# Performance work log

Hardware: AMD Instinct MI355X
Metric: run time of the kernel (lower is better)

Reference implementation:

```python
import jax, jax.numpy as jnp
import numpy as np

TOTAL_WORDS = 10000
EMBED = 100
SEQ = 80
UNITS = 512
BATCH = 2048


def setup_inputs() -> dict:
    key = jax.random.key(0)
    ks = jax.random.split(key, 12)
    s = lambda k, shape, fan: jax.random.normal(k, shape, jnp.float32) * (1.0 / np.sqrt(fan))
    return {
        "tokens": jax.random.randint(ks[0], (BATCH, SEQ), 0, TOTAL_WORDS),
        "emb": jax.random.normal(ks[1], (TOTAL_WORDS, EMBED), jnp.float32) * 0.05,
        "Wx0": s(ks[2], (EMBED, UNITS), EMBED), "Wh0": s(ks[3], (UNITS, UNITS), UNITS), "b0": jnp.zeros((UNITS,), jnp.float32),
        "Wx1": s(ks[4], (UNITS, UNITS), UNITS), "Wh1": s(ks[5], (UNITS, UNITS), UNITS), "b1": jnp.zeros((UNITS,), jnp.float32),
        "Wx2": s(ks[6], (UNITS, UNITS), UNITS), "Wh2": s(ks[7], (UNITS, UNITS), UNITS), "b2": jnp.zeros((UNITS,), jnp.float32),
        "Wout": s(ks[8], (UNITS, 1), UNITS), "bout": jnp.zeros((1,), jnp.float32),
    }


def reference(tokens, emb, Wx0, Wh0, b0, Wx1, Wh1, b1, Wx2, Wh2, b2, Wout, bout):
    # embedding lookup: [B, S, E]
    x = emb[tokens]
    xs = jnp.swapaxes(x, 0, 1)  # [S, B, E] for scan over time
    B = tokens.shape[0]
    h0 = jnp.zeros((B, UNITS), jnp.float32)
    init = (h0, h0, h0)

    def step(carry, word):
        s0, s1, s2 = carry
        o0 = jnp.tanh(word @ Wx0 + s0 @ Wh0 + b0)
        o1 = jnp.tanh(o0 @ Wx1 + s1 @ Wh1 + b1)
        o2 = jnp.tanh(o1 @ Wx2 + s2 @ Wh2 + b2)
        return (o0, o1, o2), None

    (s0, s1, s2), _ = jax.lax.scan(step, init, xs)
    logits = s2 @ Wout + bout  # [B, 1]
    return jax.nn.sigmoid(logits)
```

## Files before the change

kernel.cpp:

```cpp
#include <hip/hip_runtime.h>

#define TW    10000
#define EMBD  100
#define SEQ   80
#define U     512
#define BATCH 2048
#define RPB   16
#define NBLK  (BATCH / RPB)
#define NTHR  1024

typedef short short8 __attribute__((ext_vector_type(8)));
typedef float f32x4 __attribute__((ext_vector_type(4)));

static __device__ __forceinline__ unsigned short f2bf(float f){
  unsigned int u = __float_as_uint(f);
  u += 0x7fffu + ((u >> 16) & 1u);
  return (unsigned short)(u >> 16);
}
static __device__ __forceinline__ float bf2f(unsigned short h){
  return __uint_as_float(((unsigned int)h) << 16);
}
static __device__ __forceinline__ float fast_tanh(float x){
  float e = __expf(2.0f * x);
  return 1.0f - 2.0f / (e + 1.0f);
}

__global__ void proj_kernel(const float* __restrict__ emb, const float* __restrict__ Wx0,
                            const float* __restrict__ b0, float* __restrict__ proj){
  __shared__ float es[16][EMBD];
  const int w0 = blockIdx.x * 16;
  for (int i = threadIdx.x; i < 16 * EMBD; i += 256)
    es[i / EMBD][i % EMBD] = emb[(size_t)w0 * EMBD + i];
  __syncthreads();
  const int n = threadIdx.x;
  float accA[16], accB[16];
#pragma unroll
  for (int wi = 0; wi < 16; ++wi){ accA[wi] = 0.0f; accB[wi] = 0.0f; }
  for (int e = 0; e < EMBD; ++e){
    const float wv0 = Wx0[(size_t)e * U + n];
    const float wv1 = Wx0[(size_t)e * U + n + 256];
#pragma unroll
    for (int wi = 0; wi < 16; ++wi){
      accA[wi] += es[wi][e] * wv0;
      accB[wi] += es[wi][e] * wv1;
    }
  }
  const float bb0 = b0[n], bb1 = b0[n + 256];
  for (int wi = 0; wi < 16; ++wi){
    proj[(size_t)(w0 + wi) * U + n]       = accA[wi] + bb0;
    proj[(size_t)(w0 + wi) * U + n + 256] = accB[wi] + bb1;
  }
}

__global__ void pack_frag(const float* __restrict__ src, unsigned short* __restrict__ dst,
                          int K, int kOff, int NCH){
  const int idx = blockIdx.x * 256 + threadIdx.x;
  if (idx >= K * 512) return;
  const int k = idx / 512, n = idx % 512;
  const int wid = n >> 5, t = (n >> 4) & 1, c = n & 15;
  const int kk = k + kOff;
  const int ch = kk >> 5, khi = (kk >> 3) & 3, j = kk & 7;
  const size_t di = (size_t)wid * NCH * 1024 + (size_t)ch * 1024
                  + (size_t)t * 512 + (size_t)(khi * 16 + c) * 8 + j;
  dst[di] = f2bf(src[(size_t)k * 512 + n]);
}

template<int NCH>
static __device__ __forceinline__ void run_segment(
    const unsigned short* __restrict__ Wp,
    unsigned lofs,
    const unsigned short* __restrict__ stA0, const unsigned short* __restrict__ stA1,
    int aBase, int aSwz, f32x4* acc)
{
#pragma unroll 8
  for (int ch = 0; ch < NCH; ++ch){
    const unsigned short* sA = (NCH == 16 || ch < 16) ? stA0 : stA1;
    short8 a  = *reinterpret_cast<const short8*>(&sA[(aBase + (ch & 15) * 32) ^ aSwz]);
    short8 b0 = *reinterpret_cast<const short8*>(Wp + (unsigned)(ch * 1024) + lofs);
    short8 b1 = *reinterpret_cast<const short8*>(Wp + (unsigned)(ch * 1024 + 512) + lofs);
    acc[0] = __builtin_amdgcn_mfma_f32_16x16x32_bf16(a, b0, acc[0], 0, 0, 0);
    acc[1] = __builtin_amdgcn_mfma_f32_16x16x32_bf16(a, b1, acc[1], 0, 0, 0);
  }
}

__global__ __launch_bounds__(NTHR, 4)
void rnn_persist(const int* __restrict__ tokens,
                 const float* __restrict__ proj,
                 const unsigned short* __restrict__ P0,
                 const unsigned short* __restrict__ P1,
                 const unsigned short* __restrict__ P2,
                 const float* __restrict__ b1,
                 const float* __restrict__ b2,
                 const float* __restrict__ Wout,
                 const float* __restrict__ bout,
                 float* __restrict__ out)
{
  __shared__ unsigned short st0[RPB * U];
  __shared__ unsigned short st1[RPB * U];
  __shared__ unsigned short st2[RPB * U];

  const int tid = threadIdx.x;
  for (int i = tid; i < RPB * U; i += NTHR){ st0[i] = 0; st1[i] = 0; st2[i] = 0; }
  __syncthreads();

  const int lane = tid & 63;
  const int wid  = tid >> 6;
  const int l15  = lane & 15;
  const int khi  = lane >> 4;
  const int n0   = wid * 32;
  const int rowbase = blockIdx.x * RPB;

  const int aBase = l15 * U + khi * 8;
  const int aSwz  = (l15 & 7) << 3;

  const unsigned short* w0p = P0 + (size_t)wid * 16 * 1024;
  const unsigned short* w1p = P1 + (size_t)wid * 32 * 1024;
  const unsigned short* w2p = P2 + (size_t)wid * 32 * 1024;
  const unsigned lofs = (unsigned)lane * 8;

  const int col0 = n0 + l15;
  const int col1 = n0 + 16 + l15;
  const float b1v0 = b1[col0], b1v1 = b1[col1];
  const float b2v0 = b2[col0], b2v1 = b2[col1];

  f32x4 acc[2];

  for (int t = 0; t < SEQ; ++t){
    acc[0] = 0.0f; acc[1] = 0.0f;
    run_segment<16>(w0p, lofs, st0, st0, aBase, aSwz, acc);
    __syncthreads();
    {
      const int rr0 = khi * 4;
#pragma unroll
      for (int j = 0; j < 4; ++j){
        const int rr = rr0 + j;
        const int tk = tokens[(size_t)(rowbase + rr) * SEQ + t];
        const float z0 = acc[0][j] + proj[(size_t)tk * U + col0];
        const float z1 = acc[1][j] + proj[(size_t)tk * U + col1];
        st0[(rr * U + col0) ^ ((rr & 7) << 3)] = f2bf(fast_tanh(z0));
        st0[(rr * U + col1) ^ ((rr & 7) << 3)] = f2bf(fast_tanh(z1));
      }
    }
    __syncthreads();

    acc[0] = 0.0f; acc[1] = 0.0f;
    run_segment<32>(w1p, lofs, st0, st1, aBase, aSwz, acc);
    __syncthreads();
    {
      const int rr0 = khi * 4;
#pragma unroll
      for (int j = 0; j < 4; ++j){
        const int rr = rr0 + j;
        st1[(rr * U + col0) ^ ((rr & 7) << 3)] = f2bf(fast_tanh(acc[0][j] + b1v0));
        st1[(rr * U + col1) ^ ((rr & 7) << 3)] = f2bf(fast_tanh(acc[1][j] + b1v1));
      }
    }
    __syncthreads();

    acc[0] = 0.0f; acc[1] = 0.0f;
    run_segment<32>(w2p, lofs, st1, st2, aBase, aSwz, acc);
    __syncthreads();
    {
      const int rr0 = khi * 4;
#pragma unroll
      for (int j = 0; j < 4; ++j){
        const int rr = rr0 + j;
        st2[(rr * U + col0) ^ ((rr & 7) << 3)] = f2bf(fast_tanh(acc[0][j] + b2v0));
        st2[(rr * U + col1) ^ ((rr & 7) << 3)] = f2bf(fast_tanh(acc[1][j] + b2v1));
      }
    }
    __syncthreads();
  }

  if (wid < RPB){
    const int r = wid;
    float v = 0.0f;
#pragma unroll
    for (int jj = 0; jj < 8; ++jj){
      const int n = lane + jj * 64;
      v += bf2f(st2[(r * U + n) ^ ((r & 7) << 3)]) * Wout[n];
    }
#pragma unroll
    for (int off = 32; off > 0; off >>= 1)
      v += __shfl_down(v, off, 64);
    if (lane == 0)
      out[rowbase + r] = 1.0f / (1.0f + __expf(-(v + bout[0])));
  }
}

extern "C" void kernel_launch(void* const* d_in, const int* in_sizes, int n_in,
                              void* d_out, int out_size, void* d_ws, size_t ws_size,
                              hipStream_t stream){
  (void)in_sizes; (void)n_in; (void)out_size; (void)ws_size;
  const int*   tokens = (const int*)  d_in[0];
  const float* emb  = (const float*)d_in[1];
  const float* Wx0  = (const float*)d_in[2];
  const float* Wh0  = (const float*)d_in[3];
  const float* b0   = (const float*)d_in[4];
  const float* Wx1  = (const float*)d_in[5];
  const float* Wh1  = (const float*)d_in[6];
  const float* b1   = (const float*)d_in[7];
  const float* Wx2  = (const float*)d_in[8];
  const float* Wh2  = (const float*)d_in[9];
  const float* b2   = (const float*)d_in[10];
  const float* Wout = (const float*)d_in[11];
  const float* bout = (const float*)d_in[12];

  char* ws = (char*)d_ws;
  float* proj = (float*)ws;
  unsigned short* P0 = (unsigned short*)(ws + (size_t)TW * U * 4);
  unsigned short* P1 = P0 + (size_t)16 * 16 * 1024;
  unsigned short* P2 = P1 + (size_t)16 * 32 * 1024;

  proj_kernel<<<TW / 16, 256, 0, stream>>>(emb, Wx0, b0, proj);
  const int pblk = (U * U + 255) / 256;
  pack_frag<<<pblk, 256, 0, stream>>>(Wh0, P0, U, 0, 16);
  pack_frag<<<pblk, 256, 0, stream>>>(Wx1, P1, U, 0, 32);
  pack_frag<<<pblk, 256, 0, stream>>>(Wh1, P1, U, U, 32);
  pack_frag<<<pblk, 256, 0, stream>>>(Wx2, P2, U, 0, 32);
  pack_frag<<<pblk, 256, 0, stream>>>(Wh2, P2, U, U, 32);

  rnn_persist<<<NBLK, NTHR, 0, stream>>>(tokens, proj, P0, P1, P2,
                                         b1, b2, Wout, bout, (float*)d_out);
}
```

Measured before the change: 1.796 ms.

## Double-buffer recurrent state in LDS to cut barriers per timestep

Each layer's hidden state gets ping-pong LDS buffers (read the previous step's buffer, write the other), moved to dynamic shared memory. This drops the per-timestep barriers from six to two, since writes no longer race with reads of the same buffer. Token and embedding-projection gathers are issued before the layer-0 MFMA loop so their global latency overlaps with compute. It doubles LDS use to 96KB per block, which is allowed by raising the max dynamic shared memory attribute.

```diff
diff --git a/kernel.cpp b/kernel.cpp
--- a/kernel.cpp
+++ b/kernel.cpp
@@ -95,12 +95,10 @@
                  const float* __restrict__ bout,
                  float* __restrict__ out)
 {
-  __shared__ unsigned short st0[RPB * U];
-  __shared__ unsigned short st1[RPB * U];
-  __shared__ unsigned short st2[RPB * U];
+  extern __shared__ unsigned short smem[];
 
   const int tid = threadIdx.x;
-  for (int i = tid; i < RPB * U; i += NTHR){ st0[i] = 0; st1[i] = 0; st2[i] = 0; }
+  for (int i = tid; i < 6 * 8192; i += NTHR) smem[i] = 0;
   __syncthreads();
 
   const int lane = tid & 63;
@@ -122,63 +120,75 @@
   const int col1 = n0 + 16 + l15;
   const float b1v0 = b1[col0], b1v1 = b1[col1];
   const float b2v0 = b2[col0], b2v1 = b2[col1];
+  const int rr0 = khi * 4;
 
   f32x4 acc[2];
 
   for (int t = 0; t < SEQ; ++t){
+    const int c = t & 1;
+    unsigned short* s0r = smem + (0 + c)     * 8192;
+    unsigned short* s0w = smem + (0 + (c^1)) * 8192;
+    unsigned short* s1r = smem + (2 + c)     * 8192;
+    unsigned short* s1w = smem + (2 + (c^1)) * 8192;
+    unsigned short* s2r = smem + (4 + c)     * 8192;
+    unsigned short* s2w = smem + (4 + (c^1)) * 8192;
+
+    const int tk0 = tokens[(size_t)(rowbase + rr0 + 0) * SEQ + t];
+    const int tk1 = tokens[(size_t)(rowbase + rr0 + 1) * SEQ + t];
+    const int tk2 = tokens[(size_t)(rowbase + rr0 + 2) * SEQ + t];
+    const int tk3 = tokens[(size_t)(rowbase + rr0 + 3) * SEQ + t];
+    const float pj00 = proj[(size_t)tk0 * U + col0];
+    const float pj01 = proj[(size_t)tk1 * U + col0];
+    const float pj02 = proj[(size_t)tk2 * U + col0];
+    const float pj03 = proj[(size_t)tk3 * U + col0];
+    const float pj10 = proj[(size_t)tk0 * U + col1];
+    const float pj11 = proj[(size_t)tk1 * U + col1];
+    const float pj12 = proj[(size_t)tk2 * U + col1];
+    const float pj13 = proj[(size_t)tk3 * U + col1];
+
     acc[0] = 0.0f; acc[1] = 0.0f;
-    run_segment<16>(w0p, lofs, st0, st0, aBase, aSwz, acc);
+    run_segment<16>(w0p, lofs, s0r, s0r, aBase, aSwz, acc);
+    {
+      s0w[((rr0 + 0) * U + col0) ^ (((rr0 + 0) & 7) << 3)] = f2bf(fast_tanh(acc[0][0] + pj00));
+      s0w[((rr0 + 1) * U + col0) ^ (((rr0 + 1) & 7) << 3)] = f2bf(fast_tanh(acc[0][1] + pj01));
+      s0w[((rr0 + 2) * U + col0) ^ (((rr0 + 2) & 7) << 3)] = f2bf(fast_tanh(acc[0][2] + pj02));
+      s0w[((rr0 + 3) * U + col0) ^ (((rr0 + 3) & 7) << 3)] = f2bf(fast_tanh(acc[0][3] + pj03));
+      s0w[((rr0 + 0) * U + col1) ^ (((rr0 + 0) & 7) << 3)] = f2bf(fast_tanh(acc[1][0] + pj10));
+      s0w[((rr0 + 1) * U + col1) ^ (((rr0 + 1) & 7) << 3)] = f2bf(fast_tanh(acc[1][1] + pj11));
+      s0w[((rr0 + 2) * U + col1) ^ (((rr0 + 2) & 7) << 3)] = f2bf(fast_tanh(acc[1][2] + pj12));
+      s0w[((rr0 + 3) * U + col1) ^ (((rr0 + 3) & 7) << 3)] = f2bf(fast_tanh(acc[1][3] + pj13));
+    }
     __syncthreads();
-    {
-      const int rr0 = khi * 4;
-#pragma unroll
-      for (int j = 0; j < 4; ++j){
-        const int rr = rr0 + j;
-        const int tk = tokens[(size_t)(rowbase + rr) * SEQ + t];
-        const float z0 = acc[0][j] + proj[(size_t)tk * U + col0];
-        const float z1 = acc[1][j] + proj[(size_t)tk * U + col1];
-        st0[(rr * U + col0) ^ ((rr & 7) << 3)] = f2bf(fast_tanh(z0));
-        st0[(rr * U + col1) ^ ((rr & 7) << 3)] = f2bf(fast_tanh(z1));
-      }
+
+    acc[0] = 0.0f; acc[1] = 0.0f;
+    run_segment<32>(w1p, lofs, s0w, s1r, aBase, aSwz, acc);
+#pragma unroll
+    for (int j = 0; j < 4; ++j){
+      const int rr = rr0 + j;
+      s1w[(rr * U + col0) ^ ((rr & 7) << 3)] = f2bf(fast_tanh(acc[0][j] + b1v0));
+      s1w[(rr * U + col1) ^ ((rr & 7) << 3)] = f2bf(fast_tanh(acc[1][j] + b1v1));
     }
     __syncthreads();
 
     acc[0] = 0.0f; acc[1] = 0.0f;
-    run_segment<32>(w1p, lofs, st0, st1, aBase, aSwz, acc);
-    __syncthreads();
-    {
-      const int rr0 = khi * 4;
-#pragma unroll
-      for (int j = 0; j < 4; ++j){
-        const int rr = rr0 + j;
-        st1[(rr * U + col0) ^ ((rr & 7) << 3)] = f2bf(fast_tanh(acc[0][j] + b1v0));
-        st1[(rr * U + col1) ^ ((rr & 7) << 3)] = f2bf(fast_tanh(acc[1][j] + b1v1));
-      }
-    }
-    __syncthreads();
-
-    acc[0] = 0.0f; acc[1] = 0.0f;
-    run_segment<32>(w2p, lofs, st1, st2, aBase, aSwz, acc);
-    __syncthreads();
-    {
-      const int rr0 = khi * 4;
-#pragma unroll
-      for (int j = 0; j < 4; ++j){
-        const int rr = rr0 + j;
-        st2[(rr * U + col0) ^ ((rr & 7) << 3)] = f2bf(fast_tanh(acc[0][j] + b2v0));
-        st2[(rr * U + col1) ^ ((rr & 7) << 3)] = f2bf(fast_tanh(acc[1][j] + b2v1));
-      }
-    }
-    __syncthreads();
-  }
-
-  if (wid < RPB){
+    run_segment<32>(w2p, lofs, s1w, s2r, aBase, aSwz, acc);
+#pragma unroll
+    for (int j = 0; j < 4; ++j){
+      const int rr = rr0 + j;
+      s2w[(rr * U + col0) ^ ((rr & 7) << 3)] = f2bf(fast_tanh(acc[0][j] + b2v0));
+      s2w[(rr * U + col1) ^ ((rr & 7) << 3)] = f2bf(fast_tanh(acc[1][j] + b2v1));
+    }
+  }
+  __syncthreads();
+
+  {
+    const unsigned short* sf = smem + 4 * 8192;
     const int r = wid;
     float v = 0.0f;
 #pragma unroll
     for (int jj = 0; jj < 8; ++jj){
       const int n = lane + jj * 64;
-      v += bf2f(st2[(r * U + n) ^ ((r & 7) << 3)]) * Wout[n];
+      v += bf2f(sf[(r * U + n) ^ ((r & 7) << 3)]) * Wout[n];
     }
 #pragma unroll
     for (int off = 32; off > 0; off >>= 1)
@@ -220,6 +230,9 @@
   pack_frag<<<pblk, 256, 0, stream>>>(Wx2, P2, U, 0, 32);
   pack_frag<<<pblk, 256, 0, stream>>>(Wh2, P2, U, U, 32);
 
-  rnn_persist<<<NBLK, NTHR, 0, stream>>>(tokens, proj, P0, P1, P2,
-                                         b1, b2, Wout, bout, (float*)d_out);
-}
+  static const int kLds = 98304;
+  (void)hipFuncSetAttribute((const void*)rnn_persist,
+                            hipFuncAttributeMaxDynamicSharedMemorySize, kLds);
+  rnn_persist<<<NBLK, NTHR, kLds, stream>>>(tokens, proj, P0, P1, P2,
+                                            b1, b2, Wout, bout, (float*)d_out);
+}
```

After: 1.655 ms, median of 2. -7.8%, faster.

## Pipeline RNN layers across blocks with LDS-resident weight slices and global flags

Applied to the files above, without the earlier changes.

Replaces the per-batch-tile persistent kernel, which streamed all weights from global memory every step, with a 192-block layer/time wavefront pipeline. Each block owns one layer stage and a 64-column slice, keeps that weight slice resident in LDS, reads the previous hidden states from double-buffered global state buffers, and synchronises with other blocks through per-timestep atomic flags. Layers 0/1/2 can then overlap across timesteps, and weight reads move from global/L2 to LDS. In exchange it adds global-memory state traffic, spin-wait latency on the critical path, and a reliance on all 192 blocks being co-resident to avoid deadlock.

```diff
diff --git a/kernel.cpp b/kernel.cpp
--- a/kernel.cpp
+++ b/kernel.cpp
@@ -5,9 +5,7 @@
 #define SEQ   80
 #define U     512
 #define BATCH 2048
-#define RPB   16
-#define NBLK  (BATCH / RPB)
-#define NTHR  1024
+#define STATE_ELEMS (128 * 16 * 512)
 
 typedef short short8 __attribute__((ext_vector_type(8)));
 typedef float f32x4 __attribute__((ext_vector_type(4)));
@@ -52,139 +50,184 @@
   }
 }
 
-__global__ void pack_frag(const float* __restrict__ src, unsigned short* __restrict__ dst,
-                          int K, int kOff, int NCH){
+__global__ void pack_w(const float* __restrict__ src, unsigned short* __restrict__ dst,
+                       int chOff, int NCH){
   const int idx = blockIdx.x * 256 + threadIdx.x;
-  if (idx >= K * 512) return;
-  const int k = idx / 512, n = idx % 512;
-  const int wid = n >> 5, t = (n >> 4) & 1, c = n & 15;
-  const int kk = k + kOff;
-  const int ch = kk >> 5, khi = (kk >> 3) & 3, j = kk & 7;
-  const size_t di = (size_t)wid * NCH * 1024 + (size_t)ch * 1024
-                  + (size_t)t * 512 + (size_t)(khi * 16 + c) * 8 + j;
-  dst[di] = f2bf(src[(size_t)k * 512 + n]);
-}
-
-template<int NCH>
-static __device__ __forceinline__ void run_segment(
-    const unsigned short* __restrict__ Wp,
-    unsigned lofs,
-    const unsigned short* __restrict__ stA0, const unsigned short* __restrict__ stA1,
-    int aBase, int aSwz, f32x4* acc)
+  if (idx >= U * U) return;
+  const int k = idx / U, n = idx % U;
+  const int cs = n >> 6, ct = (n >> 4) & 3, cl = n & 15;
+  const int chL = (k >> 5) + chOff, khi = (k >> 3) & 3, j = k & 7;
+  const int lane = khi * 16 + cl;
+  const size_t di = ((((size_t)cs * 4 + ct) * NCH + chL) * 64 + lane) * 8 + j;
+  dst[di] = f2bf(src[(size_t)k * U + n]);
+}
+
+static __device__ __forceinline__ void waitflag(int* p, int need){
+  while (__hip_atomic_load(p, __ATOMIC_ACQUIRE, __HIP_MEMORY_SCOPE_AGENT) < need)
+    __builtin_amdgcn_s_sleep(1);
+}
+
+__global__ __launch_bounds__(1024, 4)
+void rnn_pipeline(const int* __restrict__ tokens,
+                  const float* __restrict__ proj,
+                  const unsigned short* __restrict__ W0p,
+                  const unsigned short* __restrict__ W1p,
+                  const unsigned short* __restrict__ W2p,
+                  const float* __restrict__ b1,
+                  const float* __restrict__ b2,
+                  const float* __restrict__ Wout,
+                  const float* __restrict__ bout,
+                  unsigned short* __restrict__ s0,
+                  unsigned short* __restrict__ s1,
+                  unsigned short* __restrict__ s2,
+                  int* __restrict__ flags,
+                  float* __restrict__ out)
 {
-#pragma unroll 8
-  for (int ch = 0; ch < NCH; ++ch){
-    const unsigned short* sA = (NCH == 16 || ch < 16) ? stA0 : stA1;
-    short8 a  = *reinterpret_cast<const short8*>(&sA[(aBase + (ch & 15) * 32) ^ aSwz]);
-    short8 b0 = *reinterpret_cast<const short8*>(Wp + (unsigned)(ch * 1024) + lofs);
-    short8 b1 = *reinterpret_cast<const short8*>(Wp + (unsigned)(ch * 1024 + 512) + lofs);
-    acc[0] = __builtin_amdgcn_mfma_f32_16x16x32_bf16(a, b0, acc[0], 0, 0, 0);
-    acc[1] = __builtin_amdgcn_mfma_f32_16x16x32_bf16(a, b1, acc[1], 0, 0, 0);
-  }
-}
-
-__global__ __launch_bounds__(NTHR, 4)
-void rnn_persist(const int* __restrict__ tokens,
-                 const float* __restrict__ proj,
-                 const unsigned short* __restrict__ P0,
-                 const unsigned short* __restrict__ P1,
-                 const unsigned short* __restrict__ P2,
-                 const float* __restrict__ b1,
-                 const float* __restrict__ b2,
-                 const float* __restrict__ Wout,
-                 const float* __restrict__ bout,
-                 float* __restrict__ out)
-{
-  __shared__ unsigned short st0[RPB * U];
-  __shared__ unsigned short st1[RPB * U];
-  __shared__ unsigned short st2[RPB * U];
-
-  const int tid = threadIdx.x;
-  for (int i = tid; i < RPB * U; i += NTHR){ st0[i] = 0; st1[i] = 0; st2[i] = 0; }
-  __syncthreads();
-
+  extern __shared__ unsigned char sm[];
+  unsigned short* wlds = (unsigned short*)sm;
+  unsigned short* exch = (unsigned short*)(sm + 131072);
+
+  const int bid   = blockIdx.x;
+  const int r     = bid & 7;
+  const int q     = bid >> 3;
+  const int stage = q >> 3;
+  const int cs    = q & 7;
+
+  const int tid  = threadIdx.x;
   const int lane = tid & 63;
   const int wid  = tid >> 6;
   const int l15  = lane & 15;
   const int khi  = lane >> 4;
-  const int n0   = wid * 32;
-  const int rowbase = blockIdx.x * RPB;
-
-  const int aBase = l15 * U + khi * 8;
-  const int aSwz  = (l15 & 7) << 3;
-
-  const unsigned short* w0p = P0 + (size_t)wid * 16 * 1024;
-  const unsigned short* w1p = P1 + (size_t)wid * 32 * 1024;
-  const unsigned short* w2p = P2 + (size_t)wid * 32 * 1024;
-  const unsigned lofs = (unsigned)lane * 8;
-
-  const int col0 = n0 + l15;
-  const int col1 = n0 + 16 + l15;
-  const float b1v0 = b1[col0], b1v1 = b1[col1];
-  const float b2v0 = b2[col0], b2v1 = b2[col1];
-
-  f32x4 acc[2];
+
+  const int NCH = (stage == 0) ? 16 : 32;
+
+  {
+    const unsigned short* wsrc =
+      (stage == 0 ? W0p : (stage == 1 ? W1p : W2p)) + (size_t)cs * 4 * NCH * 512;
+    const int n8 = 4 * NCH * 512 / 8;
+    for (int i = tid; i < n8; i += 1024)
+      *reinterpret_cast<short8*>(&wlds[(size_t)i * 8]) =
+        *reinterpret_cast<const short8*>(&wsrc[(size_t)i * 8]);
+  }
+
+  const int rt0 = (wid >> 1) * 2, rt1 = rt0 + 1;
+  const int ct0 = (wid & 1) * 2,  ct1 = ct0 + 1;
+  const int rtG0 = r * 16 + rt0,  rtG1 = r * 16 + rt1;
+
+  const int colL0 = ct0 * 16 + l15, colL1 = ct1 * 16 + l15;
+  const int colG0 = cs * 64 + colL0, colG1 = cs * 64 + colL1;
+
+  float bv0 = 0.0f, bv1 = 0.0f;
+  if (stage == 1){ bv0 = b1[colG0]; bv1 = b1[colG1]; }
+  if (stage == 2){ bv0 = b2[colG0]; bv1 = b2[colG1]; }
+
+  unsigned short* outBase = (stage == 0) ? s0 : (stage == 1 ? s1 : s2);
+
+  __syncthreads();
 
   for (int t = 0; t < SEQ; ++t){
-    acc[0] = 0.0f; acc[1] = 0.0f;
-    run_segment<16>(w0p, lofs, st0, st0, aBase, aSwz, acc);
-    __syncthreads();
-    {
-      const int rr0 = khi * 4;
-#pragma unroll
-      for (int j = 0; j < 4; ++j){
-        const int rr = rr0 + j;
-        const int tk = tokens[(size_t)(rowbase + rr) * SEQ + t];
-        const float z0 = acc[0][j] + proj[(size_t)tk * U + col0];
-        const float z1 = acc[1][j] + proj[(size_t)tk * U + col1];
-        st0[(rr * U + col0) ^ ((rr & 7) << 3)] = f2bf(fast_tanh(z0));
-        st0[(rr * U + col1) ^ ((rr & 7) << 3)] = f2bf(fast_tanh(z1));
+    const int pw = t & 1, pr = pw ^ 1;
+
+    if (tid == 0){
+      if (stage == 0){
+        if (t >= 1) waitflag(&flags[(0 * SEQ + t - 1) * 8 + r], 8);
+        if (t >= 2) waitflag(&flags[(1 * SEQ + t - 2) * 8 + r], 8);
+      } else if (stage == 1){
+        waitflag(&flags[(0 * SEQ + t) * 8 + r], 8);
+        if (t >= 1) waitflag(&flags[(1 * SEQ + t - 1) * 8 + r], 8);
+        if (t >= 2) waitflag(&flags[(2 * SEQ + t - 2) * 8 + r], 8);
+      } else {
+        waitflag(&flags[(1 * SEQ + t) * 8 + r], 8);
+        if (t >= 1) waitflag(&flags[(2 * SEQ + t - 1) * 8 + r], 8);
       }
     }
     __syncthreads();
 
-    acc[0] = 0.0f; acc[1] = 0.0f;
-    run_segment<32>(w1p, lofs, st0, st1, aBase, aSwz, acc);
-    __syncthreads();
-    {
-      const int rr0 = khi * 4;
-#pragma unroll
-      for (int j = 0; j < 4; ++j){
-        const int rr = rr0 + j;
-        st1[(rr * U + col0) ^ ((rr & 7) << 3)] = f2bf(fast_tanh(acc[0][j] + b1v0));
-        st1[(rr * U + col1) ^ ((rr & 7) << 3)] = f2bf(fast_tanh(acc[1][j] + b1v1));
+    const unsigned short* bufLow =
+      (stage == 0) ? s0 + (size_t)pr * STATE_ELEMS :
+      (stage == 1) ? s0 + (size_t)pw * STATE_ELEMS :
+                     s1 + (size_t)pw * STATE_ELEMS;
+    const unsigned short* bufHigh =
+      (stage == 0) ? bufLow :
+      (stage == 1) ? s1 + (size_t)pr * STATE_ELEMS :
+                     s2 + (size_t)pr * STATE_ELEMS;
+
+    f32x4 a00 = 0.0f, a01 = 0.0f, a10 = 0.0f, a11 = 0.0f;
+
+#pragma unroll 4
+    for (int ch = 0; ch < NCH; ++ch){
+      const unsigned short* ab = (ch < 16) ? bufLow : bufHigh;
+      const int chL = ch & 15;
+      short8 A0 = *reinterpret_cast<const short8*>(ab + ((size_t)(rtG0 * 16 + chL) * 64 + lane) * 8);
+      short8 A1 = *reinterpret_cast<const short8*>(ab + ((size_t)(rtG1 * 16 + chL) * 64 + lane) * 8);
+      short8 B0 = *reinterpret_cast<const short8*>(wlds + ((size_t)(ct0 * NCH + ch) * 64 + lane) * 8);
+      short8 B1 = *reinterpret_cast<const short8*>(wlds + ((size_t)(ct1 * NCH + ch) * 64 + lane) * 8);
+      a00 = __builtin_amdgcn_mfma_f32_16x16x32_bf16(A0, B0, a00, 0, 0, 0);
+      a01 = __builtin_amdgcn_mfma_f32_16x16x32_bf16(A0, B1, a01, 0, 0, 0);
+      a10 = __builtin_amdgcn_mfma_f32_16x16x32_bf16(A1, B0, a10, 0, 0, 0);
+      a11 = __builtin_amdgcn_mfma_f32_16x16x32_bf16(A1, B1, a11, 0, 0, 0);
+    }
+
+    const int g0 = colL0 >> 3, g1 = colL1 >> 3, j0 = colL0 & 7, j1 = colL1 & 7;
+#pragma unroll
+    for (int h = 0; h < 2; ++h){
+      const int rtL = h ? rt1 : rt0;
+      const f32x4 accA = h ? a10 : a00;
+      const f32x4 accB = h ? a11 : a01;
+#pragma unroll
+      for (int g = 0; g < 4; ++g){
+        const int rowL = rtL * 16 + khi * 4 + g;
+        float z0, z1;
+        if (stage == 0){
+          const int tok = tokens[(size_t)(r * 256 + rowL) * SEQ + t];
+          z0 = accA[g] + proj[(size_t)tok * U + colG0];
+          z1 = accB[g] + proj[(size_t)tok * U + colG1];
+        } else {
+          z0 = accA[g] + bv0;
+          z1 = accB[g] + bv1;
+        }
+        const int sw = rowL & 7;
+        exch[rowL * 64 + ((g0 ^ sw) << 3) + j0] = f2bf(fast_tanh(z0));
+        exch[rowL * 64 + ((g1 ^ sw) << 3) + j1] = f2bf(fast_tanh(z1));
       }
     }
     __syncthreads();
 
-    acc[0] = 0.0f; acc[1] = 0.0f;
-    run_segment<32>(w2p, lofs, st1, st2, aBase, aSwz, acc);
-    __syncthreads();
-    {
-      const int rr0 = khi * 4;
-#pragma unroll
-      for (int j = 0; j < 4; ++j){
-        const int rr = rr0 + j;
-        st2[(rr * U + col0) ^ ((rr & 7) << 3)] = f2bf(fast_tanh(acc[0][j] + b2v0));
-        st2[(rr * U + col1) ^ ((rr & 7) << 3)] = f2bf(fast_tanh(acc[1][j] + b2v1));
-      }
-    }
-    __syncthreads();
-  }
-
-  if (wid < RPB){
-    const int r = wid;
+    unsigned short* ob = outBase + (size_t)pw * STATE_ELEMS;
+#pragma unroll
+    for (int u = 0; u < 2; ++u){
+      const int un  = wid * 2 + u;
+      const int rtL = un >> 1;
+      const int che = un & 1;
+      const int rowE = rtL * 16 + l15;
+      const int gg = che * 4 + khi;
+      short8 v = *reinterpret_cast<const short8*>(&exch[rowE * 64 + ((gg ^ (rowE & 7)) << 3)]);
+      *reinterpret_cast<short8*>(ob + ((size_t)((r * 16 + rtL) * 16 + (cs * 2 + che)) * 64 + lane) * 8) = v;
+    }
+    __syncthreads();
+
+    if (tid == 0)
+      __hip_atomic_fetch_add(&flags[(stage * SEQ + t) * 8 + r], 1,
+                             __ATOMIC_RELEASE, __HIP_MEMORY_SCOPE_AGENT);
+  }
+
+  if (stage == 2 && cs == 0){
+    if (tid == 0) waitflag(&flags[(2 * SEQ + SEQ - 1) * 8 + r], 8);
+    __syncthreads();
+    const unsigned short* sf = s2 + (size_t)((SEQ - 1) & 1) * STATE_ELEMS;
+    const int rtG = r * 16 + wid;
     float v = 0.0f;
 #pragma unroll
-    for (int jj = 0; jj < 8; ++jj){
-      const int n = lane + jj * 64;
-      v += bf2f(st2[(r * U + n) ^ ((r & 7) << 3)]) * Wout[n];
-    }
-#pragma unroll
-    for (int off = 32; off > 0; off >>= 1)
-      v += __shfl_down(v, off, 64);
-    if (lane == 0)
-      out[rowbase + r] = 1.0f / (1.0f + __expf(-(v + bout[0])));
+    for (int ch = 0; ch < 16; ++ch){
+      short8 a = *reinterpret_cast<const short8*>(sf + ((size_t)(rtG * 16 + ch) * 64 + lane) * 8);
+      const float* wp = Wout + ch * 32 + khi * 8;
+#pragma unroll
+      for (int j = 0; j < 8; ++j) v += bf2f((unsigned short)a[j]) * wp[j];
+    }
+    v += __shfl_xor(v, 16, 64);
+    v += __shfl_xor(v, 32, 64);
+    if (lane < 16)
+      out[r * 256 + wid * 16 + lane] = 1.0f / (1.0f + __expf(-(v + bout[0])));
   }
 }
 
@@ -208,18 +251,31 @@
 
   char* ws = (char*)d_ws;
   float* proj = (float*)ws;
-  unsigned short* P0 = (unsigned short*)(ws + (size_t)TW * U * 4);
-  unsigned short* P1 = P0 + (size_t)16 * 16 * 1024;
-  unsigned short* P2 = P1 + (size_t)16 * 32 * 1024;
+  unsigned short* W0p = (unsigned short*)(ws + 20480000);
+  unsigned short* W1p = (unsigned short*)(ws + 21004288);
+  unsigned short* W2p = (unsigned short*)(ws + 22052864);
+  unsigned short* s0  = (unsigned short*)(ws + 23101440);
+  unsigned short* s1  = (unsigned short*)(ws + 27295744);
+  unsigned short* s2  = (unsigned short*)(ws + 31490048);
+  int* flags          = (int*)(ws + 35684352);
+
+  hipMemsetAsync(s0 + STATE_ELEMS, 0, (size_t)STATE_ELEMS * 2, stream);
+  hipMemsetAsync(s1 + STATE_ELEMS, 0, (size_t)STATE_ELEMS * 2, stream);
+  hipMemsetAsync(s2 + STATE_ELEMS, 0, (size_t)STATE_ELEMS * 2, stream);
+  hipMemsetAsync(flags, 0, 3 * SEQ * 8 * sizeof(int), stream);
 
   proj_kernel<<<TW / 16, 256, 0, stream>>>(emb, Wx0, b0, proj);
   const int pblk = (U * U + 255) / 256;
-  pack_frag<<<pblk, 256, 0, stream>>>(Wh0, P0, U, 0, 16);
-  pack_frag<<<pblk, 256, 0, stream>>>(Wx1, P1, U, 0, 32);
-  pack_frag<<<pblk, 256, 0, stream>>>(Wh1, P1, U, U, 32);
-  pack_frag<<<pblk, 256, 0, stream>>>(Wx2, P2, U, 0, 32);
-  pack_frag<<<pblk, 256, 0, stream>>>(Wh2, P2, U, U, 32);
-
-  rnn_persist<<<NBLK, NTHR, 0, stream>>>(tokens, proj, P0, P1, P2,
-                                         b1, b2, Wout, bout, (float*)d_out);
-}
+  pack_w<<<pblk, 256, 0, stream>>>(Wh0, W0p, 0, 16);
+  pack_w<<<pblk, 256, 0, stream>>>(Wx1, W1p, 0, 32);
+  pack_w<<<pblk, 256, 0, stream>>>(Wh1, W1p, 16, 32);
+  pack_w<<<pblk, 256, 0, stream>>>(Wx2, W2p, 0, 32);
+  pack_w<<<pblk, 256, 0, stream>>>(Wh2, W2p, 16, 32);
+
+  static const int kLds = 163840;
+  (void)hipFuncSetAttribute((const void*)rnn_pipeline,
+                            hipFuncAttributeMaxDynamicSharedMemorySize, kLds);
+  rnn_pipeline<<<192, 1024, kLds, stream>>>(tokens, proj, W0p, W1p, W2p,
+                                            b1, b2, Wout, bout,
+                                            s0, s1, s2, flags, (float*)d_out);
+}
```

After: 1.931 ms. 7.5% more time.
